# Performance work log

Measured on AMD Instinct MI355X. Metric: run time of the kernel, lower is better.

Reference implementation:

```python
import jax, jax.numpy as jnp
import numpy as np

S, B, H = 2048, 2, 1024
NH = 16
HD = H // NH  # 64


def setup_inputs() -> dict:
    key = jax.random.key(0)
    k1, k2 = jax.random.split(key)
    hidden_states = jax.random.normal(k1, (S, B, H), dtype=jnp.float32)
    W_qkv = jax.random.normal(k2, (3 * H, H), dtype=jnp.float32) * (H ** -0.5)
    b_qkv = jnp.zeros((3 * H,), dtype=jnp.float32)
    return {"hidden_states": hidden_states, "W_qkv": W_qkv, "b_qkv": b_qkv}


def reference(hidden_states, W_qkv, b_qkv):
    s, b, h = hidden_states.shape
    # QKV projection: [S,B,3H] -> [S,B,NH,3*HD] -> split
    qkv = hidden_states @ W_qkv.T + b_qkv
    qkv = qkv.reshape(s, b, NH, 3 * HD)
    q, k, v = jnp.split(qkv, 3, axis=-1)  # each [S,B,NH,HD]
    norm_factor = HD ** -0.5
    # scores: [B,NH,Sq,Sk]
    scores = jnp.einsum('sbhd,tbhd->bhst', q, k) * norm_factor
    # Cumsum sequence-op (seq_op_in_fp32=True): cumsum over key dim, scaled by Sq^-0.5
    probs = jnp.cumsum(scores.astype(jnp.float32), axis=-1) * (s ** -0.5)
    probs = probs.astype(hidden_states.dtype)
    # PV: [B,NH,Sq,HD] -> seq-first [Sq,B,NH*HD]
    ctx = jnp.einsum('bhst,tbhd->sbhd', probs, v)
    return ctx.reshape(s, b, h)
```

## Files before the change

kernel.cpp:

```cpp
#include <hip/hip_runtime.h>

#define S 2048
#define B 2
#define H 1024
#define NH 16
#define HD 64
#define THREE_H 3072
#define ROWS (S*B)

typedef __attribute__((ext_vector_type(8))) short short8;
typedef __attribute__((ext_vector_type(4))) float f32x4;
typedef const __attribute__((address_space(1))) unsigned int* gptr_t;
typedef __attribute__((address_space(3))) unsigned int* lptr_t;

#define N8_A (ROWS * H / 8)
#define N8_W (THREE_H * H / 8)

__device__ __forceinline__ ushort f2bf(float f) {
    union { float f; unsigned u; } v; v.f = f;
    unsigned r = v.u + 0x7fffu + ((v.u >> 16) & 1u);
    return (ushort)(r >> 16);
}
__device__ __forceinline__ float bf2f(ushort u) {
    union { unsigned u; float f; } v; v.u = ((unsigned)u) << 16;
    return v.f;
}

__global__ void cast_both(const float* __restrict__ A, const float* __restrict__ W,
                          ushort* __restrict__ Ab, ushort* __restrict__ Wb) {
    int i = blockIdx.x * 256 + threadIdx.x;
    const float4* s4;
    ushort* dst;
    if (i < N8_A) { s4 = (const float4*)A; dst = Ab; }
    else if (i < N8_A + N8_W) { s4 = (const float4*)W; dst = Wb; i -= N8_A; }
    else return;
    float4 a = s4[2 * i], b = s4[2 * i + 1];
    short8 o;
    o[0] = f2bf(a.x); o[1] = f2bf(a.y); o[2] = f2bf(a.z); o[3] = f2bf(a.w);
    o[4] = f2bf(b.x); o[5] = f2bf(b.y); o[6] = f2bf(b.z); o[7] = f2bf(b.w);
    *(short8*)(dst + 8 * (size_t)i) = o;
}

__global__ __launch_bounds__(512) void qkv_gemm_mfma(const ushort* __restrict__ Abf,
                                                     const ushort* __restrict__ Wbf,
                                                     const float* __restrict__ bias,
                                                     ushort* __restrict__ Qb,
                                                     ushort* __restrict__ Ktd,
                                                     ushort* __restrict__ Vtd) {
    __shared__ ushort Abuf[128 * 32];
    __shared__ ushort Bbuf[128 * 32];
    const int tid = threadIdx.x;
    const int wave = tid >> 6, lane = tid & 63;
    const int wr = wave >> 1, wc = wave & 1;
    const int row0 = blockIdx.x * 128;
    const int col0 = blockIdx.y * 128;

    f32x4 acc[2][4] = {};

    const int lrow = lane >> 2;
    const int gk = ((lane & 3) ^ ((lrow >> 1) & 3)) * 8;
    const int il = lane & 15, ko = lane >> 4;

    for (int k0 = 0; k0 < H; k0 += 32) {
        {
            int row = wave * 16 + lrow;
            __builtin_amdgcn_global_load_lds(
                (gptr_t)&Abf[(size_t)(row0 + row) * H + k0 + gk],
                (lptr_t)&Abuf[wave * 512 + lane * 8], 16, 0, 0);
            __builtin_amdgcn_global_load_lds(
                (gptr_t)&Wbf[(size_t)(col0 + row) * H + k0 + gk],
                (lptr_t)&Bbuf[wave * 512 + lane * 8], 16, 0, 0);
        }
        __syncthreads();

        short8 af[2], bfr[4];
#pragma unroll
        for (int m = 0; m < 2; ++m) {
            int ar = wr * 32 + m * 16 + il;
            af[m] = *(const short8*)&Abuf[ar * 32 + (ko ^ ((ar >> 1) & 3)) * 8];
        }
#pragma unroll
        for (int n = 0; n < 4; ++n) {
            int br = wc * 64 + n * 16 + il;
            bfr[n] = *(const short8*)&Bbuf[br * 32 + (ko ^ ((br >> 1) & 3)) * 8];
        }
#pragma unroll
        for (int m = 0; m < 2; ++m)
#pragma unroll
            for (int n = 0; n < 4; ++n)
                acc[m][n] = __builtin_amdgcn_mfma_f32_16x16x32_bf16(af[m], bfr[n], acc[m][n], 0, 0, 0);
        __syncthreads();
    }

#pragma unroll
    for (int n = 0; n < 4; ++n) {
        int cbase = col0 + wc * 64 + n * 16;
        int h   = cbase / 192;
        int r3  = cbase % 192;
        int sel = r3 >> 6;
        int d   = (r3 & 63) + il;
        float bv = bias[cbase + il];
        if (sel == 0) {
#pragma unroll
            for (int m = 0; m < 2; ++m) {
                int rowb = row0 + wr * 32 + m * 16 + ko * 4;
#pragma unroll
                for (int j = 0; j < 4; ++j) {
                    int r = rowb + j;
                    int s = r >> 1, b = r & 1;
                    Qb[((size_t)((b * NH + h) * S + s)) * HD + d] = f2bf(acc[m][n][j] + bv);
                }
            }
        } else {
            ushort* dst = (sel == 1) ? Ktd : Vtd;
            const size_t ro0 = ((size_t)(h)      * HD + d) * S;
            const size_t ro1 = ((size_t)(NH + h) * HD + d) * S;
#pragma unroll
            for (int m = 0; m < 2; ++m) {
                int t0 = (row0 + wr * 32 + m * 16 + ko * 4) >> 1;
                uint lo = (uint)f2bf(acc[m][n][0] + bv) |
                          ((uint)f2bf(acc[m][n][2] + bv) << 16);
                uint hi = (uint)f2bf(acc[m][n][1] + bv) |
                          ((uint)f2bf(acc[m][n][3] + bv) << 16);
                *(uint*)&dst[ro0 + t0] = lo;
                *(uint*)&dst[ro1 + t0] = hi;
            }
        }
    }
}

__global__ __launch_bounds__(256) void vscan(ushort* __restrict__ Vtd) {
    const int row = blockIdx.x * 4 + (threadIdx.x >> 6);
    const int lane = threadIdx.x & 63;
    ushort* vp = Vtd + (size_t)row * S + lane * 32;
    float v[32];
#pragma unroll
    for (int q = 0; q < 4; ++q) {
        short8 x = *(const short8*)(vp + q * 8);
#pragma unroll
        for (int k = 0; k < 8; ++k) v[q * 8 + k] = bf2f((ushort)x[k]);
    }
    float sum = 0.f;
#pragma unroll
    for (int k = 0; k < 32; ++k) sum += v[k];
    float t = sum;
#pragma unroll
    for (int off = 1; off < 64; off <<= 1) {
        float o = __shfl_down(t, off, 64);
        if (lane + off < 64) t += o;
    }
    float acc = t - sum;
#pragma unroll
    for (int k = 31; k >= 0; --k) { acc += v[k]; v[k] = acc; }
#pragma unroll
    for (int q = 0; q < 4; ++q) {
        short8 o;
#pragma unroll
        for (int k = 0; k < 8; ++k) o[k] = f2bf(v[q * 8 + k]);
        *(short8*)(vp + q * 8) = o;
    }
}

__global__ __launch_bounds__(512) void kvqm_fused(const ushort* __restrict__ Kt,
                                                  const ushort* __restrict__ Vt,
                                                  const ushort* __restrict__ Qb,
                                                  float* __restrict__ out) {
    __shared__ float red[4][4096];
    __shared__ ushort Mt[64][72];
    const int bh = blockIdx.x, sb = blockIdx.y;
    const int b = bh >> 4, h = bh & 15;
    const int tid = threadIdx.x, wave = tid >> 6, lane = tid & 63;
    const int il = lane & 15, g = lane >> 4;
    const ushort* Kp = Kt + (size_t)bh * HD * S;
    const ushort* Vp = Vt + (size_t)bh * HD * S;

    f32x4 acc[4][4] = {};
    {
        const int tbase = wave * 256 + g * 8;
#pragma unroll
        for (int ks = 0; ks < 8; ++ks) {
            const int t = tbase + ks * 32;
            short8 af[4], bfv[4];
#pragma unroll
            for (int m = 0; m < 4; ++m) af[m]  = *(const short8*)&Kp[(size_t)(m * 16 + il) * S + t];
#pragma unroll
            for (int n = 0; n < 4; ++n) bfv[n] = *(const short8*)&Vp[(size_t)(n * 16 + il) * S + t];
#pragma unroll
            for (int m = 0; m < 4; ++m)
#pragma unroll
                for (int n = 0; n < 4; ++n)
                    acc[m][n] = __builtin_amdgcn_mfma_f32_16x16x32_bf16(af[m], bfv[n], acc[m][n], 0, 0, 0);
        }
    }

#define DUMP(dstbuf)                                                        \
    { float* _d = (dstbuf);                                                 \
      _Pragma("unroll") for (int m = 0; m < 4; ++m)                         \
      _Pragma("unroll") for (int n = 0; n < 4; ++n)                         \
      _Pragma("unroll") for (int j = 0; j < 4; ++j)                         \
          _d[(m * 16 + g * 4 + j) * 64 + n * 16 + il] = acc[m][n][j]; }
#define ADDIN(srcbuf)                                                       \
    { const float* _s = (srcbuf);                                           \
      _Pragma("unroll") for (int m = 0; m < 4; ++m)                         \
      _Pragma("unroll") for (int n = 0; n < 4; ++n)                         \
      _Pragma("unroll") for (int j = 0; j < 4; ++j)                         \
          acc[m][n][j] += _s[(m * 16 + g * 4 + j) * 64 + n * 16 + il]; }
    if (wave >= 4) DUMP(red[wave - 4]);
    __syncthreads();
    if (wave < 4) ADDIN(red[wave]);
    __syncthreads();
    if (wave == 2 || wave == 3) DUMP(red[wave - 2]);
    __syncthreads();
    if (wave < 2) ADDIN(red[wave]);
    __syncthreads();
    if (wave == 1) DUMP(red[0]);
    __syncthreads();
    if (wave == 0) {
        ADDIN(red[0]);
#pragma unroll
        for (int m = 0; m < 4; ++m)
#pragma unroll
            for (int n = 0; n < 4; ++n)
#pragma unroll
                for (int j = 0; j < 4; ++j)
                    Mt[n * 16 + il][m * 16 + g * 4 + j] = f2bf(acc[m][n][j]);
    }
    __syncthreads();
#undef DUMP
#undef ADDIN

    const int s0b = sb * 256 + wave * 32;
    f32x4 qacc[2][4] = {};
#pragma unroll
    for (int ks = 0; ks < 2; ++ks) {
        short8 af[2], bfv[4];
#pragma unroll
        for (int m = 0; m < 2; ++m) {
            int s = s0b + m * 16 + il;
            af[m] = *(const short8*)&Qb[((size_t)bh * S + s) * HD + ks * 32 + g * 8];
        }
#pragma unroll
        for (int n = 0; n < 4; ++n)
            bfv[n] = *(const short8*)&Mt[n * 16 + il][ks * 32 + g * 8];
#pragma unroll
        for (int m = 0; m < 2; ++m)
#pragma unroll
            for (int n = 0; n < 4; ++n)
                qacc[m][n] = __builtin_amdgcn_mfma_f32_16x16x32_bf16(af[m], bfv[n], qacc[m][n], 0, 0, 0);
    }
    const float scale = 0.125f * 0.02209708691207961f;
#pragma unroll
    for (int m = 0; m < 2; ++m)
#pragma unroll
        for (int n = 0; n < 4; ++n)
#pragma unroll
            for (int j = 0; j < 4; ++j) {
                int s = s0b + m * 16 + g * 4 + j;
                int d = n * 16 + il;
                out[(size_t)(s * B + b) * H + h * 64 + d] = qacc[m][n][j] * scale;
            }
}

extern "C" void kernel_launch(void* const* d_in, const int* in_sizes, int n_in,
                              void* d_out, int out_size, void* d_ws, size_t ws_size,
                              hipStream_t stream) {
    const float* hidden = (const float*)d_in[0];
    const float* W      = (const float*)d_in[1];
    const float* bias   = (const float*)d_in[2];
    float* out = (float*)d_out;

    ushort* Qb    = (ushort*)d_ws;
    ushort* Ktd   = Qb + 4194304;
    ushort* Vtd   = Ktd + 4194304;
    ushort* Abf   = Vtd + 4194304;
    ushort* Wbf   = Abf + 4194304;

    cast_both<<<(N8_A + N8_W + 255) / 256, 256, 0, stream>>>(hidden, W, Abf, Wbf);
    qkv_gemm_mfma<<<dim3(ROWS / 128, THREE_H / 128), 512, 0, stream>>>(Abf, Wbf, bias, Qb, Ktd, Vtd);
    vscan<<<512, 256, 0, stream>>>(Vtd);
    kvqm_fused<<<dim3(32, 8), 512, 0, stream>>>(Ktd, Vtd, Qb, out);
}
```

Measured before the change: 77.00 us.

## Split fused KV/QM kernel to compute K^T V once per head

```diff
diff --git a/kernel.cpp b/kernel.cpp
--- a/kernel.cpp
+++ b/kernel.cpp
@@ -161,14 +161,11 @@
     }
 }
 
-__global__ __launch_bounds__(512) void kvqm_fused(const ushort* __restrict__ Kt,
+__global__ __launch_bounds__(512) void kvm_single(const ushort* __restrict__ Kt,
                                                   const ushort* __restrict__ Vt,
-                                                  const ushort* __restrict__ Qb,
-                                                  float* __restrict__ out) {
+                                                  ushort* __restrict__ Mg) {
     __shared__ float red[4][4096];
-    __shared__ ushort Mt[64][72];
-    const int bh = blockIdx.x, sb = blockIdx.y;
-    const int b = bh >> 4, h = bh & 15;
+    const int bh = blockIdx.x;
     const int tid = threadIdx.x, wave = tid >> 6, lane = tid & 63;
     const int il = lane & 15, g = lane >> 4;
     const ushort* Kp = Kt + (size_t)bh * HD * S;
@@ -192,7 +189,6 @@
                     acc[m][n] = __builtin_amdgcn_mfma_f32_16x16x32_bf16(af[m], bfv[n], acc[m][n], 0, 0, 0);
         }
     }
-
 #define DUMP(dstbuf)                                                        \
     { float* _d = (dstbuf);                                                 \
       _Pragma("unroll") for (int m = 0; m < 4; ++m)                         \
@@ -217,47 +213,65 @@
     __syncthreads();
     if (wave == 0) {
         ADDIN(red[0]);
+        ushort* Mp = Mg + (size_t)bh * 4096;
 #pragma unroll
         for (int m = 0; m < 4; ++m)
 #pragma unroll
             for (int n = 0; n < 4; ++n)
 #pragma unroll
                 for (int j = 0; j < 4; ++j)
-                    Mt[n * 16 + il][m * 16 + g * 4 + j] = f2bf(acc[m][n][j]);
-    }
-    __syncthreads();
+                    Mp[(n * 16 + il) * 64 + m * 16 + g * 4 + j] = f2bf(acc[m][n][j]);
+    }
 #undef DUMP
 #undef ADDIN
-
-    const int s0b = sb * 256 + wave * 32;
-    f32x4 qacc[2][4] = {};
+}
+
+__global__ __launch_bounds__(256) void qm_mfma(const ushort* __restrict__ Qb,
+                                               const ushort* __restrict__ Mg,
+                                               float* __restrict__ out) {
+    __shared__ ushort Mt[64][72];
+    const int bh = blockIdx.x, b = bh >> 4, h = bh & 15;
+    const int tid = threadIdx.x;
+    {
+        const int e0 = tid * 16;
+        const ushort* src = Mg + (size_t)bh * 4096 + e0;
+        short8 x0 = *(const short8*)(src);
+        short8 x1 = *(const short8*)(src + 8);
+        *(short8*)&Mt[e0 >> 6][e0 & 63] = x0;
+        *(short8*)&Mt[e0 >> 6][(e0 & 63) + 8] = x1;
+    }
+    __syncthreads();
+    const int wave = tid >> 6, lane = tid & 63;
+    const int sl15 = lane & 15, koct = (lane >> 4) * 8;
+    const int s0b = blockIdx.y * 256 + wave * 64;
+    f32x4 acc[4][4] = {};
 #pragma unroll
     for (int ks = 0; ks < 2; ++ks) {
-        short8 af[2], bfv[4];
-#pragma unroll
-        for (int m = 0; m < 2; ++m) {
-            int s = s0b + m * 16 + il;
-            af[m] = *(const short8*)&Qb[((size_t)bh * S + s) * HD + ks * 32 + g * 8];
+        short8 af[4], bfv[4];
+#pragma unroll
+        for (int m = 0; m < 4; ++m) {
+            int s = s0b + m * 16 + sl15;
+            af[m] = *(const short8*)&Qb[((size_t)bh * S + s) * HD + ks * 32 + koct];
         }
 #pragma unroll
         for (int n = 0; n < 4; ++n)
-            bfv[n] = *(const short8*)&Mt[n * 16 + il][ks * 32 + g * 8];
-#pragma unroll
-        for (int m = 0; m < 2; ++m)
+            bfv[n] = *(const short8*)&Mt[n * 16 + sl15][ks * 32 + koct];
+#pragma unroll
+        for (int m = 0; m < 4; ++m)
 #pragma unroll
             for (int n = 0; n < 4; ++n)
-                qacc[m][n] = __builtin_amdgcn_mfma_f32_16x16x32_bf16(af[m], bfv[n], qacc[m][n], 0, 0, 0);
+                acc[m][n] = __builtin_amdgcn_mfma_f32_16x16x32_bf16(af[m], bfv[n], acc[m][n], 0, 0, 0);
     }
     const float scale = 0.125f * 0.02209708691207961f;
 #pragma unroll
-    for (int m = 0; m < 2; ++m)
+    for (int m = 0; m < 4; ++m)
 #pragma unroll
         for (int n = 0; n < 4; ++n)
 #pragma unroll
             for (int j = 0; j < 4; ++j) {
-                int s = s0b + m * 16 + g * 4 + j;
-                int d = n * 16 + il;
-                out[(size_t)(s * B + b) * H + h * 64 + d] = qacc[m][n][j] * scale;
+                int s = s0b + m * 16 + (lane >> 4) * 4 + j;
+                int d = n * 16 + sl15;
+                out[(size_t)(s * B + b) * H + h * 64 + d] = acc[m][n][j] * scale;
             }
 }
 
@@ -272,11 +286,13 @@
     ushort* Qb    = (ushort*)d_ws;
     ushort* Ktd   = Qb + 4194304;
     ushort* Vtd   = Ktd + 4194304;
-    ushort* Abf   = Vtd + 4194304;
+    ushort* Mg    = Vtd + 4194304;
+    ushort* Abf   = Mg + 131072;
     ushort* Wbf   = Abf + 4194304;
 
     cast_both<<<(N8_A + N8_W + 255) / 256, 256, 0, stream>>>(hidden, W, Abf, Wbf);
     qkv_gemm_mfma<<<dim3(ROWS / 128, THREE_H / 128), 512, 0, stream>>>(Abf, Wbf, bias, Qb, Ktd, Vtd);
     vscan<<<512, 256, 0, stream>>>(Vtd);
-    kvqm_fused<<<dim3(32, 8), 512, 0, stream>>>(Ktd, Vtd, Qb, out);
-}
+    kvm_single<<<32, 512, 0, stream>>>(Ktd, Vtd, Mg);
+    qm_mfma<<<dim3(32, 8), 256, 0, stream>>>(Qb, Mg, out);
+}
```

Result: slower. 79.07 us (+2.7%).
